# Performance work log

Measured on AMD Instinct MI355X. Metric: run time of the kernel, lower is better.

Reference implementation:

```python
import jax, jax.numpy as jnp
import numpy as np

B, S, F, H, L = 4096, 512, 8, 10, 2


def setup_inputs() -> dict:
    key = jax.random.key(0)
    ks = jax.random.split(key, 12)
    bound = 1.0 / np.sqrt(H)  # PyTorch LSTM/Linear init scale
    u = lambda k, shape: jax.random.uniform(k, shape, jnp.float32, -bound, bound)
    return {
        "input_tensor": jax.random.normal(ks[0], (B, S, F), jnp.float32),
        "hidden": jnp.zeros((L, B, H), jnp.float32),
        "cell": jnp.zeros((L, B, H), jnp.float32),
        # layer 0 (input size F), layer 1 (input size H); gate order i,f,g,o
        "W_ih0": u(ks[1], (4 * H, F)), "W_hh0": u(ks[2], (4 * H, H)),
        "b_ih0": u(ks[3], (4 * H,)),   "b_hh0": u(ks[4], (4 * H,)),
        "W_ih1": u(ks[5], (4 * H, H)), "W_hh1": u(ks[6], (4 * H, H)),
        "b_ih1": u(ks[7], (4 * H,)),   "b_hh1": u(ks[8], (4 * H,)),
        "W_fc": u(ks[9], (1, H)),      "b_fc": u(ks[10], (1,)),
    }


def _lstm_layer(x_sbf, h0, c0, W_ih, W_hh, b_ih, b_hh):
    # x_sbf: [S, B, Fin]; h0,c0: [B, H]. Returns hs [S,B,H], (hT, cT).
    b = b_ih + b_hh

    def step(carry, x):
        h, c = carry
        gates = x @ W_ih.T + h @ W_hh.T + b  # [B, 4H]
        i, f, g, o = jnp.split(gates, 4, axis=-1)
        c = jax.nn.sigmoid(f) * c + jax.nn.sigmoid(i) * jnp.tanh(g)
        h = jax.nn.sigmoid(o) * jnp.tanh(c)
        return (h, c), h

    (hT, cT), hs = jax.lax.scan(step, (h0, c0), x_sbf)
    return hs, hT, cT


def reference(input_tensor, hidden, cell,
              W_ih0, W_hh0, b_ih0, b_hh0,
              W_ih1, W_hh1, b_ih1, b_hh1,
              W_fc, b_fc):
    x = jnp.transpose(input_tensor, (1, 0, 2))  # [S, B, F]
    hs0, h0T, c0T = _lstm_layer(x, hidden[0], cell[0], W_ih0, W_hh0, b_ih0, b_hh0)
    hs1, h1T, c1T = _lstm_layer(hs0, hidden[1], cell[1], W_ih1, W_hh1, b_ih1, b_hh1)
    out = hs1[-1]                      # last timestep, [B, H]
    out_regression = out @ W_fc.T + b_fc  # [B, 1]
    hidden_out = jnp.stack([h0T, h1T])
    cell_out = jnp.stack([c0T, c1T])
    return out_regression, hidden_out, cell_out
```

## Files before the change

kernel.cpp:

```cpp
#include <hip/hip_runtime.h>


typedef __fp16 v2h __attribute__((ext_vector_type(2)));

#define L2E 1.4426950408889634f

#define HAS_FDOT2 __has_builtin(__builtin_amdgcn_fdot2)

__device__ __forceinline__ v2h pkh(float a, float b) {
    return __builtin_amdgcn_cvt_pkrtz(a, b);
}

#define SIGM(a)  __builtin_amdgcn_rcpf(1.0f + __builtin_amdgcn_exp2f(-(a)))
#define TANHP(a) fmaf(-2.0f, __builtin_amdgcn_rcpf(1.0f + __builtin_amdgcn_exp2f(a)), 1.0f)

#if HAS_FDOT2
#define DOT2(acc, w, v) (acc) = __builtin_amdgcn_fdot2((w), (v), (acc), false)
#else
#define DOT2(acc, w, v) (acc) = fmaf((float)(w).x, (float)(v).x, fmaf((float)(w).y, (float)(v).y, (acc)))
#endif

__global__ __launch_bounds__(256, 2)
void lstm2_r6(const float* __restrict__ x,
              const float* __restrict__ hid,
              const float* __restrict__ cel,
              const float* __restrict__ Wih0, const float* __restrict__ Whh0,
              const float* __restrict__ bih0, const float* __restrict__ bhh0,
              const float* __restrict__ Wih1, const float* __restrict__ Whh1,
              const float* __restrict__ bih1, const float* __restrict__ bhh1,
              const float* __restrict__ Wfc,  const float* __restrict__ bfc,
              float* __restrict__ out)
{
    __shared__ __fp16 h0buf[8][8][16];
    __shared__ __fp16 h1buf[8][16];

    const int tid  = threadIdx.x;
    const int wid  = tid >> 6;
    const int uwid = __builtin_amdgcn_readfirstlane(wid);
    const int l16  = tid & 15;
    const int grp  = (tid & 63) >> 4;
    const int eIB  = ((wid & 1) << 2) + grp;
    const int e    = blockIdx.x * 8 + eIB;
    const int j    = (l16 < 10) ? l16 : 0;
    const bool act = (l16 < 10);

    if (uwid < 2) {
        v2h wA[4][5], wx[4][4];  float bb[4];
        #pragma unroll
        for (int g = 0; g < 4; ++g) {
            const int r = g * 10 + j;
            const float sc = (g == 2) ? 2.0f * L2E : L2E;
            #pragma unroll
            for (int k = 0; k < 5; ++k) wA[g][k] = pkh(Whh0[r*10 + 2*k] * sc, Whh0[r*10 + 2*k+1] * sc);
            #pragma unroll
            for (int k = 0; k < 4; ++k) wx[g][k] = pkh(Wih0[r*8 + 2*k] * sc, Wih0[r*8 + 2*k+1] * sc);
            bb[g] = (bih0[r] + bhh0[r]) * sc;
        }
        v2h hv[5];
        #pragma unroll
        for (int k = 0; k < 5; ++k) hv[k] = pkh(hid[e*10 + 2*k], hid[e*10 + 2*k+1]);
        float cc = cel[e * 10 + j];
        float hj = 0.0f;

        __fp16* const wbase = &h0buf[0][eIB][0];

        const float4* __restrict__ xp = reinterpret_cast<const float4*>(x + (size_t)e * 4096);
        float4 xb0[2], xb1[2], xb2[2], xb3[2];
        xb0[0] = xp[0]; xb0[1] = xp[1];
        xb1[0] = xp[2]; xb1[1] = xp[3];
        xb2[0] = xp[4]; xb2[1] = xp[5];
        xb3[0] = xp[6]; xb3[1] = xp[7];

#define L0STEP(XB, S, TN)                                                    \
        {                                                                    \
            v2h xh0 = pkh(XB[0].x, XB[0].y), xh1 = pkh(XB[0].z, XB[0].w);    \
            v2h xh2 = pkh(XB[1].x, XB[1].y), xh3 = pkh(XB[1].z, XB[1].w);    \
            { int tn = (TN) > 511 ? 511 : (TN);                              \
              XB[0] = xp[2*tn]; XB[1] = xp[2*tn + 1]; }                      \
            float a0 = bb[0], a1 = bb[1], a2 = bb[2], a3 = bb[3];            \
            DOT2(a0, wx[0][0], xh0); DOT2(a1, wx[1][0], xh0);                \
            DOT2(a2, wx[2][0], xh0); DOT2(a3, wx[3][0], xh0);                \
            DOT2(a0, wx[0][1], xh1); DOT2(a1, wx[1][1], xh1);                \
            DOT2(a2, wx[2][1], xh1); DOT2(a3, wx[3][1], xh1);                \
            DOT2(a0, wx[0][2], xh2); DOT2(a1, wx[1][2], xh2);                \
            DOT2(a2, wx[2][2], xh2); DOT2(a3, wx[3][2], xh2);                \
            DOT2(a0, wx[0][3], xh3); DOT2(a1, wx[1][3], xh3);                \
            DOT2(a2, wx[2][3], xh3); DOT2(a3, wx[3][3], xh3);                \
            _Pragma("unroll")                                                \
            for (int k = 0; k < 5; ++k) {                                    \
                DOT2(a0, wA[0][k], hv[k]); DOT2(a1, wA[1][k], hv[k]);        \
                DOT2(a2, wA[2][k], hv[k]); DOT2(a3, wA[3][k], hv[k]);        \
            }                                                                \
            float i_ = SIGM(a0), f_ = SIGM(a1);                              \
            float g_ = TANHP(a2), o_ = SIGM(a3);                             \
            cc = fmaf(f_, cc, i_ * g_);                                      \
            float tc_ = (2.0f * L2E) * cc;                                   \
            hj = o_ * TANHP(tc_);                                            \
            wbase[(S)*128 + l16] = (__fp16)hj;                               \
            { const v2h* rb_ = (const v2h*)(wbase + (S)*128);                \
              hv[0] = rb_[0]; hv[1] = rb_[1]; hv[2] = rb_[2];                \
              hv[3] = rb_[3]; hv[4] = rb_[4]; }                              \
        }

        for (int it = 0; it < 64; ++it) {
            const int tb = 8 * it;
            L0STEP(xb0, 0, tb + 4)
            L0STEP(xb1, 1, tb + 5)
            L0STEP(xb2, 2, tb + 6)
            L0STEP(xb3, 3, tb + 7)
            __syncthreads();
            L0STEP(xb0, 4, tb + 8)
            L0STEP(xb1, 5, tb + 9)
            L0STEP(xb2, 6, tb + 10)
            L0STEP(xb3, 7, tb + 11)
            __syncthreads();
        }
#undef L0STEP

        if (act) {
            out[4096          + e * 10 + l16] = hj;
            out[4096 + 81920  + e * 10 + l16] = cc;
        }

    } else {
        v2h wA[4][5], wB[4][5];  float bb[4];
        #pragma unroll
        for (int g = 0; g < 4; ++g) {
            const int r = g * 10 + j;
            const float sc = (g == 2) ? 2.0f * L2E : L2E;
            #pragma unroll
            for (int k = 0; k < 5; ++k) wA[g][k] = pkh(Whh1[r*10 + 2*k] * sc, Whh1[r*10 + 2*k+1] * sc);
            #pragma unroll
            for (int k = 0; k < 5; ++k) wB[g][k] = pkh(Wih1[r*10 + 2*k] * sc, Wih1[r*10 + 2*k+1] * sc);
            bb[g] = (bih1[r] + bhh1[r]) * sc;
        }
        const float wfc = act ? Wfc[j] : 0.0f;
        v2h hv[5];
        #pragma unroll
        for (int k = 0; k < 5; ++k) hv[k] = pkh(hid[40960 + e*10 + 2*k], hid[40960 + e*10 + 2*k+1]);
        float cc = cel[40960 + e * 10 + j];
        float hj = 0.0f;

        __fp16* const h1w = &h1buf[eIB][0];
        const __fp16* const rbase = &h0buf[0][eIB][0];

#define L1STEP(S)                                                            \
        {                                                                    \
            const v2h* ir_ = (const v2h*)(rbase + (S)*128);                  \
            v2h i0_ = ir_[0], i1_ = ir_[1], i2_ = ir_[2],                    \
                i3_ = ir_[3], i4_ = ir_[4];                                  \
            float a0 = bb[0], a1 = bb[1], a2 = bb[2], a3 = bb[3];            \
            _Pragma("unroll")                                                \
            for (int k = 0; k < 5; ++k) {                                    \
                DOT2(a0, wA[0][k], hv[k]); DOT2(a1, wA[1][k], hv[k]);        \
                DOT2(a2, wA[2][k], hv[k]); DOT2(a3, wA[3][k], hv[k]);        \
            }                                                                \
            DOT2(a0, wB[0][0], i0_); DOT2(a1, wB[1][0], i0_);                \
            DOT2(a2, wB[2][0], i0_); DOT2(a3, wB[3][0], i0_);                \
            DOT2(a0, wB[0][1], i1_); DOT2(a1, wB[1][1], i1_);                \
            DOT2(a2, wB[2][1], i1_); DOT2(a3, wB[3][1], i1_);                \
            DOT2(a0, wB[0][2], i2_); DOT2(a1, wB[1][2], i2_);                \
            DOT2(a2, wB[2][2], i2_); DOT2(a3, wB[3][2], i2_);                \
            DOT2(a0, wB[0][3], i3_); DOT2(a1, wB[1][3], i3_);                \
            DOT2(a2, wB[2][3], i3_); DOT2(a3, wB[3][3], i3_);                \
            DOT2(a0, wB[0][4], i4_); DOT2(a1, wB[1][4], i4_);                \
            DOT2(a2, wB[2][4], i4_); DOT2(a3, wB[3][4], i4_);                \
            float i_ = SIGM(a0), f_ = SIGM(a1);                              \
            float g_ = TANHP(a2), o_ = SIGM(a3);                             \
            cc = fmaf(f_, cc, i_ * g_);                                      \
            float tc_ = (2.0f * L2E) * cc;                                   \
            hj = o_ * TANHP(tc_);                                            \
            h1w[l16] = (__fp16)hj;                                           \
            { const v2h* rb_ = (const v2h*)h1w;                              \
              hv[0] = rb_[0]; hv[1] = rb_[1]; hv[2] = rb_[2];                \
              hv[3] = rb_[3]; hv[4] = rb_[4]; }                              \
        }

        for (int it = 0; it < 64; ++it) {
            __syncthreads();
            L1STEP(0)
            L1STEP(1)
            L1STEP(2)
            L1STEP(3)
            __syncthreads();
            L1STEP(4)
            L1STEP(5)
            L1STEP(6)
            L1STEP(7)
        }
#undef L1STEP

        float p = hj * wfc;
        #pragma unroll
        for (int off = 8; off > 0; off >>= 1) p += __shfl_xor(p, off, 16);
        if (l16 == 0) out[e] = p + bfc[0];
        if (act) {
            out[4096 + 40960  + e * 10 + l16] = hj;
            out[4096 + 122880 + e * 10 + l16] = cc;
        }
    }
}

extern "C" void kernel_launch(void* const* d_in, const int* in_sizes, int n_in,
                              void* d_out, int out_size, void* d_ws, size_t ws_size,
                              hipStream_t stream) {
    const float* x    = (const float*)d_in[0];
    const float* hid  = (const float*)d_in[1];
    const float* cel  = (const float*)d_in[2];
    const float* Wih0 = (const float*)d_in[3];
    const float* Whh0 = (const float*)d_in[4];
    const float* bih0 = (const float*)d_in[5];
    const float* bhh0 = (const float*)d_in[6];
    const float* Wih1 = (const float*)d_in[7];
    const float* Whh1 = (const float*)d_in[8];
    const float* bih1 = (const float*)d_in[9];
    const float* bhh1 = (const float*)d_in[10];
    const float* Wfc  = (const float*)d_in[11];
    const float* bfc  = (const float*)d_in[12];

    hipLaunchKernelGGL(lstm2_r6, dim3(512), dim3(256), 0, stream,
                       x, hid, cel, Wih0, Whh0, bih0, bhh0,
                       Wih1, Whh1, bih1, bhh1, Wfc, bfc,
                       (float*)d_out);
}
```

Measured before the change: 181.8 us.

## Split LSTM gates across 20-lane groups with bpermute exchange, 6 sequences per block

Each batch element now uses 20 lanes instead of 16: each lane computes two gate pre-activations, (i,g) or (f,o), rather than all four. The f and o activations are passed to the unit lanes with ds_bpermute. This halves the serial dot-product chain per step and packs 3 elements per wave, so fewer lanes sit idle, at the cost of a cross-lane permute per step and a larger grid of 683 blocks with a tail guard. The final FC reduction moves from shuffles to a shared-memory sum.

```diff
diff --git a/kernel.cpp b/kernel.cpp
--- a/kernel.cpp
+++ b/kernel.cpp
@@ -4,24 +4,21 @@
 typedef __fp16 v2h __attribute__((ext_vector_type(2)));
 
 #define L2E 1.4426950408889634f
-
-#define HAS_FDOT2 __has_builtin(__builtin_amdgcn_fdot2)
 
 __device__ __forceinline__ v2h pkh(float a, float b) {
     return __builtin_amdgcn_cvt_pkrtz(a, b);
 }
+__device__ __forceinline__ float bpermf(int baddr, float v) {
+    int r = __builtin_amdgcn_ds_bpermute(baddr, __builtin_bit_cast(int, v));
+    return __builtin_bit_cast(float, r);
+}
 
 #define SIGM(a)  __builtin_amdgcn_rcpf(1.0f + __builtin_amdgcn_exp2f(-(a)))
 #define TANHP(a) fmaf(-2.0f, __builtin_amdgcn_rcpf(1.0f + __builtin_amdgcn_exp2f(a)), 1.0f)
-
-#if HAS_FDOT2
 #define DOT2(acc, w, v) (acc) = __builtin_amdgcn_fdot2((w), (v), (acc), false)
-#else
-#define DOT2(acc, w, v) (acc) = fmaf((float)(w).x, (float)(v).x, fmaf((float)(w).y, (float)(v).y, (acc)))
-#endif
 
 __global__ __launch_bounds__(256, 2)
-void lstm2_r6(const float* __restrict__ x,
+void lstm2_r8(const float* __restrict__ x,
               const float* __restrict__ hid,
               const float* __restrict__ cel,
               const float* __restrict__ Wih0, const float* __restrict__ Whh0,
@@ -31,75 +28,84 @@
               const float* __restrict__ Wfc,  const float* __restrict__ bfc,
               float* __restrict__ out)
 {
-    __shared__ __fp16 h0buf[8][8][16];
-    __shared__ __fp16 h1buf[8][16];
+    __shared__ __fp16 h0buf[8][6][20];
+    __shared__ __fp16 h1buf[6][20];
+    __shared__ float  fcb[6][10];
 
     const int tid  = threadIdx.x;
+    const int lane = tid & 63;
     const int wid  = tid >> 6;
     const int uwid = __builtin_amdgcn_readfirstlane(wid);
-    const int l16  = tid & 15;
-    const int grp  = (tid & 63) >> 4;
-    const int eIB  = ((wid & 1) << 2) + grp;
-    const int e    = blockIdx.x * 8 + eIB;
-    const int j    = (l16 < 10) ? l16 : 0;
-    const bool act = (l16 < 10);
+    int grp = lane / 20;
+    int l20 = lane - grp * 20;
+    if (lane >= 60) { grp = 2; l20 = 19; }
+    const int  ju       = (l20 < 10) ? l20 : l20 - 10;
+    const bool unitlane = (l20 < 10);
+    const int  eIw = (wid & 1) * 3 + grp;
+    const int  e   = blockIdx.x * 6 + eIw;
+    const int  ec  = (e < 4095) ? e : 4095;
+    const int  baddr = ((l20 < 10) ? (lane + 10) : lane) * 4;
+
+    const float alpha2 = unitlane ? 2.0f : 1.0f;
+    const float beta2  = unitlane ? -1.0f : 0.0f;
+    const float scB    = unitlane ? 2.0f * L2E : L2E;
+    const int   rA = l20, rB = 20 + l20;
 
     if (uwid < 2) {
-        v2h wA[4][5], wx[4][4];  float bb[4];
-        #pragma unroll
-        for (int g = 0; g < 4; ++g) {
-            const int r = g * 10 + j;
-            const float sc = (g == 2) ? 2.0f * L2E : L2E;
-            #pragma unroll
-            for (int k = 0; k < 5; ++k) wA[g][k] = pkh(Whh0[r*10 + 2*k] * sc, Whh0[r*10 + 2*k+1] * sc);
-            #pragma unroll
-            for (int k = 0; k < 4; ++k) wx[g][k] = pkh(Wih0[r*8 + 2*k] * sc, Wih0[r*8 + 2*k+1] * sc);
-            bb[g] = (bih0[r] + bhh0[r]) * sc;
-        }
+        v2h wxA[4], wxB[4], whA[5], whB[5];
+        #pragma unroll
+        for (int k = 0; k < 4; ++k) {
+            wxA[k] = pkh(Wih0[rA*8+2*k]*L2E, Wih0[rA*8+2*k+1]*L2E);
+            wxB[k] = pkh(Wih0[rB*8+2*k]*scB, Wih0[rB*8+2*k+1]*scB);
+        }
+        #pragma unroll
+        for (int k = 0; k < 5; ++k) {
+            whA[k] = pkh(Whh0[rA*10+2*k]*L2E, Whh0[rA*10+2*k+1]*L2E);
+            whB[k] = pkh(Whh0[rB*10+2*k]*scB, Whh0[rB*10+2*k+1]*scB);
+        }
+        const float bA = (bih0[rA] + bhh0[rA]) * L2E;
+        const float bB = (bih0[rB] + bhh0[rB]) * scB;
+
         v2h hv[5];
         #pragma unroll
-        for (int k = 0; k < 5; ++k) hv[k] = pkh(hid[e*10 + 2*k], hid[e*10 + 2*k+1]);
-        float cc = cel[e * 10 + j];
+        for (int k = 0; k < 5; ++k) hv[k] = pkh(hid[ec*10+2*k], hid[ec*10+2*k+1]);
+        float cc = cel[ec * 10 + ju];
         float hj = 0.0f;
 
-        __fp16* const wbase = &h0buf[0][eIB][0];
-
-        const float4* __restrict__ xp = reinterpret_cast<const float4*>(x + (size_t)e * 4096);
+        __fp16* const wbase = &h0buf[0][eIw][0];
+        __fp16* const wlane = wbase + l20;
+
+        const float4* __restrict__ xp = reinterpret_cast<const float4*>(x + (size_t)ec * 4096);
         float4 xb0[2], xb1[2], xb2[2], xb3[2];
-        xb0[0] = xp[0]; xb0[1] = xp[1];
-        xb1[0] = xp[2]; xb1[1] = xp[3];
-        xb2[0] = xp[4]; xb2[1] = xp[5];
-        xb3[0] = xp[6]; xb3[1] = xp[7];
+        xb0[0]=xp[0]; xb0[1]=xp[1];  xb1[0]=xp[2]; xb1[1]=xp[3];
+        xb2[0]=xp[4]; xb2[1]=xp[5];  xb3[0]=xp[6]; xb3[1]=xp[7];
 
 #define L0STEP(XB, S, TN)                                                    \
         {                                                                    \
-            v2h xh0 = pkh(XB[0].x, XB[0].y), xh1 = pkh(XB[0].z, XB[0].w);    \
-            v2h xh2 = pkh(XB[1].x, XB[1].y), xh3 = pkh(XB[1].z, XB[1].w);    \
-            { int tn = (TN) > 511 ? 511 : (TN);                              \
-              XB[0] = xp[2*tn]; XB[1] = xp[2*tn + 1]; }                      \
-            float a0 = bb[0], a1 = bb[1], a2 = bb[2], a3 = bb[3];            \
-            DOT2(a0, wx[0][0], xh0); DOT2(a1, wx[1][0], xh0);                \
-            DOT2(a2, wx[2][0], xh0); DOT2(a3, wx[3][0], xh0);                \
-            DOT2(a0, wx[0][1], xh1); DOT2(a1, wx[1][1], xh1);                \
-            DOT2(a2, wx[2][1], xh1); DOT2(a3, wx[3][1], xh1);                \
-            DOT2(a0, wx[0][2], xh2); DOT2(a1, wx[1][2], xh2);                \
-            DOT2(a2, wx[2][2], xh2); DOT2(a3, wx[3][2], xh2);                \
-            DOT2(a0, wx[0][3], xh3); DOT2(a1, wx[1][3], xh3);                \
-            DOT2(a2, wx[2][3], xh3); DOT2(a3, wx[3][3], xh3);                \
-            _Pragma("unroll")                                                \
-            for (int k = 0; k < 5; ++k) {                                    \
-                DOT2(a0, wA[0][k], hv[k]); DOT2(a1, wA[1][k], hv[k]);        \
-                DOT2(a2, wA[2][k], hv[k]); DOT2(a3, wA[3][k], hv[k]);        \
-            }                                                                \
-            float i_ = SIGM(a0), f_ = SIGM(a1);                              \
-            float g_ = TANHP(a2), o_ = SIGM(a3);                             \
-            cc = fmaf(f_, cc, i_ * g_);                                      \
-            float tc_ = (2.0f * L2E) * cc;                                   \
-            hj = o_ * TANHP(tc_);                                            \
-            wbase[(S)*128 + l16] = (__fp16)hj;                               \
-            { const v2h* rb_ = (const v2h*)(wbase + (S)*128);                \
-              hv[0] = rb_[0]; hv[1] = rb_[1]; hv[2] = rb_[2];                \
-              hv[3] = rb_[3]; hv[4] = rb_[4]; }                              \
+            v2h x0=pkh(XB[0].x,XB[0].y), x1=pkh(XB[0].z,XB[0].w);            \
+            v2h x2=pkh(XB[1].x,XB[1].y), x3=pkh(XB[1].z,XB[1].w);            \
+            { int tn=(TN)>511?511:(TN); XB[0]=xp[2*tn]; XB[1]=xp[2*tn+1]; }  \
+            float aA = bA, aB = bB;                                          \
+            DOT2(aA,wxA[0],x0); DOT2(aB,wxB[0],x0);                          \
+            DOT2(aA,wxA[1],x1); DOT2(aB,wxB[1],x1);                          \
+            DOT2(aA,wxA[2],x2); DOT2(aB,wxB[2],x2);                          \
+            DOT2(aA,wxA[3],x3); DOT2(aB,wxB[3],x3);                          \
+            DOT2(aA,whA[0],hv[0]); DOT2(aB,whB[0],hv[0]);                    \
+            DOT2(aA,whA[1],hv[1]); DOT2(aB,whB[1],hv[1]);                    \
+            DOT2(aA,whA[2],hv[2]); DOT2(aB,whB[2],hv[2]);                    \
+            DOT2(aA,whA[3],hv[3]); DOT2(aB,whB[3],hv[3]);                    \
+            DOT2(aA,whA[4],hv[4]); DOT2(aB,whB[4],hv[4]);                    \
+            float r1 = SIGM(aA);                                             \
+            float r2 = __builtin_amdgcn_rcpf(1.0f + __builtin_amdgcn_exp2f(-aB)); \
+            float act2 = fmaf(alpha2, r2, beta2);                            \
+            float ig = r1 * act2;                                            \
+            float sf = bpermf(baddr, r1);                                    \
+            float so = bpermf(baddr, act2);                                  \
+            cc = fmaf(sf, cc, ig);                                           \
+            hj = so * TANHP((2.0f*L2E) * cc);                                \
+            wlane[(S)*120] = (__fp16)hj;                                     \
+            { const v2h* rb = (const v2h*)(wbase + (S)*120);                 \
+              hv[0]=rb[0]; hv[1]=rb[1]; hv[2]=rb[2]; hv[3]=rb[3]; hv[4]=rb[4]; } \
         }
 
         for (int it = 0; it < 64; ++it) {
@@ -117,63 +123,61 @@
         }
 #undef L0STEP
 
-        if (act) {
-            out[4096          + e * 10 + l16] = hj;
-            out[4096 + 81920  + e * 10 + l16] = cc;
+        __syncthreads();
+        if (unitlane && e < 4096) {
+            out[4096          + e * 10 + ju] = hj;
+            out[4096 + 81920  + e * 10 + ju] = cc;
         }
 
     } else {
-        v2h wA[4][5], wB[4][5];  float bb[4];
-        #pragma unroll
-        for (int g = 0; g < 4; ++g) {
-            const int r = g * 10 + j;
-            const float sc = (g == 2) ? 2.0f * L2E : L2E;
-            #pragma unroll
-            for (int k = 0; k < 5; ++k) wA[g][k] = pkh(Whh1[r*10 + 2*k] * sc, Whh1[r*10 + 2*k+1] * sc);
-            #pragma unroll
-            for (int k = 0; k < 5; ++k) wB[g][k] = pkh(Wih1[r*10 + 2*k] * sc, Wih1[r*10 + 2*k+1] * sc);
-            bb[g] = (bih1[r] + bhh1[r]) * sc;
-        }
-        const float wfc = act ? Wfc[j] : 0.0f;
+        v2h wiA[5], wiB[5], whA[5], whB[5];
+        #pragma unroll
+        for (int k = 0; k < 5; ++k) {
+            wiA[k] = pkh(Wih1[rA*10+2*k]*L2E, Wih1[rA*10+2*k+1]*L2E);
+            wiB[k] = pkh(Wih1[rB*10+2*k]*scB, Wih1[rB*10+2*k+1]*scB);
+            whA[k] = pkh(Whh1[rA*10+2*k]*L2E, Whh1[rA*10+2*k+1]*L2E);
+            whB[k] = pkh(Whh1[rB*10+2*k]*scB, Whh1[rB*10+2*k+1]*scB);
+        }
+        const float bA = (bih1[rA] + bhh1[rA]) * L2E;
+        const float bB = (bih1[rB] + bhh1[rB]) * scB;
+        const float wfc = Wfc[ju];
+
         v2h hv[5];
         #pragma unroll
-        for (int k = 0; k < 5; ++k) hv[k] = pkh(hid[40960 + e*10 + 2*k], hid[40960 + e*10 + 2*k+1]);
-        float cc = cel[40960 + e * 10 + j];
+        for (int k = 0; k < 5; ++k) hv[k] = pkh(hid[40960+ec*10+2*k], hid[40960+ec*10+2*k+1]);
+        float cc = cel[40960 + ec * 10 + ju];
         float hj = 0.0f;
 
-        __fp16* const h1w = &h1buf[eIB][0];
-        const __fp16* const rbase = &h0buf[0][eIB][0];
-
-#define L1STEP(S)                                                            \
+        const __fp16* const rbase = &h0buf[0][eIw][0];
+        __fp16* const h1w  = &h1buf[eIw][0];
+        __fp16* const h1wl = h1w + l20;
+
+#define L1STEP(SR)                                                           \
         {                                                                    \
-            const v2h* ir_ = (const v2h*)(rbase + (S)*128);                  \
-            v2h i0_ = ir_[0], i1_ = ir_[1], i2_ = ir_[2],                    \
-                i3_ = ir_[3], i4_ = ir_[4];                                  \
-            float a0 = bb[0], a1 = bb[1], a2 = bb[2], a3 = bb[3];            \
-            _Pragma("unroll")                                                \
-            for (int k = 0; k < 5; ++k) {                                    \
-                DOT2(a0, wA[0][k], hv[k]); DOT2(a1, wA[1][k], hv[k]);        \
-                DOT2(a2, wA[2][k], hv[k]); DOT2(a3, wA[3][k], hv[k]);        \
-            }                                                                \
-            DOT2(a0, wB[0][0], i0_); DOT2(a1, wB[1][0], i0_);                \
-            DOT2(a2, wB[2][0], i0_); DOT2(a3, wB[3][0], i0_);                \
-            DOT2(a0, wB[0][1], i1_); DOT2(a1, wB[1][1], i1_);                \
-            DOT2(a2, wB[2][1], i1_); DOT2(a3, wB[3][1], i1_);                \
-            DOT2(a0, wB[0][2], i2_); DOT2(a1, wB[1][2], i2_);                \
-            DOT2(a2, wB[2][2], i2_); DOT2(a3, wB[3][2], i2_);                \
-            DOT2(a0, wB[0][3], i3_); DOT2(a1, wB[1][3], i3_);                \
-            DOT2(a2, wB[2][3], i3_); DOT2(a3, wB[3][3], i3_);                \
-            DOT2(a0, wB[0][4], i4_); DOT2(a1, wB[1][4], i4_);                \
-            DOT2(a2, wB[2][4], i4_); DOT2(a3, wB[3][4], i4_);                \
-            float i_ = SIGM(a0), f_ = SIGM(a1);                              \
-            float g_ = TANHP(a2), o_ = SIGM(a3);                             \
-            cc = fmaf(f_, cc, i_ * g_);                                      \
-            float tc_ = (2.0f * L2E) * cc;                                   \
-            hj = o_ * TANHP(tc_);                                            \
-            h1w[l16] = (__fp16)hj;                                           \
-            { const v2h* rb_ = (const v2h*)h1w;                              \
-              hv[0] = rb_[0]; hv[1] = rb_[1]; hv[2] = rb_[2];                \
-              hv[3] = rb_[3]; hv[4] = rb_[4]; }                              \
+            const v2h* ir = (const v2h*)(rbase + (SR)*120);                  \
+            v2h p0=ir[0], p1=ir[1], p2=ir[2], p3=ir[3], p4=ir[4];            \
+            float aA = bA, aB = bB;                                          \
+            DOT2(aA,wiA[0],p0); DOT2(aB,wiB[0],p0);                          \
+            DOT2(aA,wiA[1],p1); DOT2(aB,wiB[1],p1);                          \
+            DOT2(aA,wiA[2],p2); DOT2(aB,wiB[2],p2);                          \
+            DOT2(aA,wiA[3],p3); DOT2(aB,wiB[3],p3);                          \
+            DOT2(aA,wiA[4],p4); DOT2(aB,wiB[4],p4);                          \
+            DOT2(aA,whA[0],hv[0]); DOT2(aB,whB[0],hv[0]);                    \
+            DOT2(aA,whA[1],hv[1]); DOT2(aB,whB[1],hv[1]);                    \
+            DOT2(aA,whA[2],hv[2]); DOT2(aB,whB[2],hv[2]);                    \
+            DOT2(aA,whA[3],hv[3]); DOT2(aB,whB[3],hv[3]);                    \
+            DOT2(aA,whA[4],hv[4]); DOT2(aB,whB[4],hv[4]);                    \
+            float r1 = SIGM(aA);                                             \
+            float r2 = __builtin_amdgcn_rcpf(1.0f + __builtin_amdgcn_exp2f(-aB)); \
+            float act2 = fmaf(alpha2, r2, beta2);                            \
+            float ig = r1 * act2;                                            \
+            float sf = bpermf(baddr, r1);                                    \
+            float so = bpermf(baddr, act2);                                  \
+            cc = fmaf(sf, cc, ig);                                           \
+            hj = so * TANHP((2.0f*L2E) * cc);                                \
+            h1wl[0] = (__fp16)hj;                                            \
+            { const v2h* rb = (const v2h*)h1w;                               \
+              hv[0]=rb[0]; hv[1]=rb[1]; hv[2]=rb[2]; hv[3]=rb[3]; hv[4]=rb[4]; } \
         }
 
         for (int it = 0; it < 64; ++it) {
@@ -190,13 +194,17 @@
         }
 #undef L1STEP
 
-        float p = hj * wfc;
-        #pragma unroll
-        for (int off = 8; off > 0; off >>= 1) p += __shfl_xor(p, off, 16);
-        if (l16 == 0) out[e] = p + bfc[0];
-        if (act) {
-            out[4096 + 40960  + e * 10 + l16] = hj;
-            out[4096 + 122880 + e * 10 + l16] = cc;
+        if (unitlane) fcb[eIw][ju] = hj * wfc;
+        __syncthreads();
+        if (l20 == 0 && e < 4096) {
+            float p = bfc[0];
+            #pragma unroll
+            for (int k = 0; k < 10; ++k) p += fcb[eIw][k];
+            out[e] = p;
+        }
+        if (unitlane && e < 4096) {
+            out[4096 + 40960  + e * 10 + ju] = hj;
+            out[4096 + 122880 + e * 10 + ju] = cc;
         }
     }
 }
@@ -218,7 +226,7 @@
     const float* Wfc  = (const float*)d_in[11];
     const float* bfc  = (const float*)d_in[12];
 
-    hipLaunchKernelGGL(lstm2_r6, dim3(512), dim3(256), 0, stream,
+    hipLaunchKernelGGL(lstm2_r8, dim3(683), dim3(256), 0, stream,
                        x, hid, cel, Wih0, Whh0, bih0, bhh0,
                        Wih1, Whh1, bih1, bhh1, Wfc, bfc,
                        (float*)d_out);
```

New measurement: 173.3 us. 1.05x faster.
